# Performance work log

Hardware: AMD Instinct MI355X
Metric: run time of the kernel (lower is better)

Reference implementation:

```python
import jax, jax.numpy as jnp
import numpy as np

B, S, D = 2, 2048, 1024
M = 2048          # d_mlp
E = 8             # num_experts
TOP_K = 2


def setup_inputs() -> dict:
    key = jax.random.key(0)
    ks = jax.random.split(key, 5)
    std = 0.02
    return {
        "residual": jax.random.normal(ks[0], (B, S, D), jnp.float32),
        "W_router": jax.random.normal(ks[1], (D, E), jnp.float32) * std,
        "W_gate": jax.random.normal(ks[2], (E, D, M), jnp.float32) * std,
        "b_gate": jnp.zeros((E, M), jnp.float32),
        "W_up": jax.random.normal(ks[3], (E, D, M), jnp.float32) * std,
        "b_up": jnp.zeros((E, M), jnp.float32),
        "W_out": jax.random.normal(ks[4], (E, M, D), jnp.float32) * std,
        "b_out": jnp.zeros((E, D), jnp.float32),
    }


def reference(residual, W_router, W_gate, b_gate, W_up, b_up, W_out, b_out):
    # --- router: softmax over experts, top-k selection, renormalize ---
    router_logits = jnp.einsum('bsd,de->bse', residual, W_router)
    router_probs = jax.nn.softmax(router_logits, axis=-1)
    top_k_probs, top_k_idx = jax.lax.top_k(router_probs, TOP_K)          # [B,S,K]
    top_k_probs = top_k_probs / (jnp.sum(top_k_probs, -1, keepdims=True) + 1e-8)
    # per-expert combine weight [B,S,E]; top-k indices are unique per token
    one_hot = jax.nn.one_hot(top_k_idx, E, dtype=residual.dtype)          # [B,S,K,E]
    expert_weights = jnp.einsum('bsk,bske->bse', top_k_probs, one_hot)
    # --- each expert runs dense SwiGLU MLP on the FULL batch (compute-then-mask, as in source) ---
    gate = jax.nn.silu(jnp.einsum('bsd,edm->ebsm', residual, W_gate) + b_gate[:, None, None, :])
    up = jnp.einsum('bsd,edm->ebsm', residual, W_up) + b_up[:, None, None, :]
    hidden = gate * up                                                    # [E,B,S,M]
    expert_out = jnp.einsum('ebsm,emd->ebsd', hidden, W_out) + b_out[:, None, None, :]
    # --- weighted combine (weights are zero for non-selected experts) ---
    output = jnp.einsum('bse,ebsd->bsd', expert_weights, expert_out)
    return output
```

## Files before the change

kernel.cpp:

```cpp
#include <hip/hip_runtime.h>
#include <cstdint>
#include <cstddef>

#define TT 4096
#define DD 1024
#define MM 2048
#define EE 8
#define NPAIR 8192

typedef unsigned short u16;
typedef __bf16 bf16x8 __attribute__((ext_vector_type(8)));
typedef float f32x4 __attribute__((ext_vector_type(4)));
typedef u16 u16x8 __attribute__((ext_vector_type(8)));
typedef __attribute__((address_space(3))) void* lds_vp;
typedef __attribute__((address_space(1))) const void* gbl_cvp;

__device__ __forceinline__ void async16(u16* l, const u16* g) {
  __builtin_amdgcn_global_load_lds((gbl_cvp)(const void*)g, (lds_vp)(void*)l, 16, 0, 0);
}

__device__ __forceinline__ u16 f2bf(float f) {
  uint32_t u = __builtin_bit_cast(uint32_t, f);
  u += 0x7fffu + ((u >> 16) & 1u);
  return (u16)(u >> 16);
}
__device__ __forceinline__ float bf2f(u16 h) {
  uint32_t u = ((uint32_t)h) << 16;
  return __builtin_bit_cast(float, u);
}

__global__ void router_kernel(const float* __restrict__ X, const float* __restrict__ Wr,
                              int* __restrict__ tok_idx, float* __restrict__ wpair,
                              u16* __restrict__ Xbf) {
  int wave = threadIdx.x >> 6;
  int lane = threadIdx.x & 63;
  int t = blockIdx.x * 4 + wave;
  const float4* x4 = (const float4*)(X + (size_t)t * DD);
  float acc[EE];
#pragma unroll
  for (int e = 0; e < EE; e++) acc[e] = 0.f;
#pragma unroll
  for (int i = 0; i < 4; i++) {
    float4 xv = x4[i * 64 + lane];
    ushort4 o;
    o.x = f2bf(xv.x); o.y = f2bf(xv.y); o.z = f2bf(xv.z); o.w = f2bf(xv.w);
    *(ushort4*)&Xbf[(size_t)t * DD + (size_t)(i * 64 + lane) * 4] = o;
    const float4* wr4 = (const float4*)(Wr + (size_t)(i * 256 + lane * 4) * EE);
    float xs[4] = {xv.x, xv.y, xv.z, xv.w};
#pragma unroll
    for (int c = 0; c < 4; c++) {
      float4 wa = wr4[c * 2 + 0];
      float4 wb = wr4[c * 2 + 1];
      acc[0] += xs[c] * wa.x; acc[1] += xs[c] * wa.y;
      acc[2] += xs[c] * wa.z; acc[3] += xs[c] * wa.w;
      acc[4] += xs[c] * wb.x; acc[5] += xs[c] * wb.y;
      acc[6] += xs[c] * wb.z; acc[7] += xs[c] * wb.w;
    }
  }
#pragma unroll
  for (int off = 32; off > 0; off >>= 1)
#pragma unroll
    for (int e = 0; e < EE; e++) acc[e] += __shfl_xor(acc[e], off);
  if (lane == 0) {
    float mx = acc[0];
#pragma unroll
    for (int e = 1; e < EE; e++) mx = fmaxf(mx, acc[e]);
    float p[EE], s = 0.f;
#pragma unroll
    for (int e = 0; e < EE; e++) { p[e] = __expf(acc[e] - mx); s += p[e]; }
    float inv = 1.f / s;
#pragma unroll
    for (int e = 0; e < EE; e++) p[e] *= inv;
    int i0 = 0;
#pragma unroll
    for (int e = 1; e < EE; e++) if (p[e] > p[i0]) i0 = e;
    int i1 = (i0 == 0) ? 1 : 0;
#pragma unroll
    for (int e = 0; e < EE; e++) if (e != i0 && p[e] > p[i1]) i1 = e;
    float denom = p[i0] + p[i1] + 1e-8f;
    tok_idx[t * 2 + 0] = i0;
    tok_idx[t * 2 + 1] = i1;
    wpair[t * 2 + 0] = p[i0] / denom;
    wpair[t * 2 + 1] = p[i1] / denom;
  }
}

__global__ void bucket_kernel(const int* __restrict__ tok_idx, int* __restrict__ offsets,
                              int* __restrict__ bucket) {
  __shared__ int lcnt[EE];
  __shared__ int lcur[EE];
  int tid = threadIdx.x;
  if (tid < EE) lcnt[tid] = 0;
  __syncthreads();
  for (int i = tid; i < NPAIR; i += 1024) atomicAdd(&lcnt[tok_idx[i]], 1);
  __syncthreads();
  if (tid == 0) {
    int s = 0;
    for (int e = 0; e < EE; e++) {
      offsets[e] = s;
      lcur[e] = s;
      s += lcnt[e];
    }
    offsets[EE] = s;
  }
  __syncthreads();
  for (int i = tid; i < NPAIR; i += 1024) {
    int e = tok_idx[i];
    int pos = atomicAdd(&lcur[e], 1);
    bucket[pos] = i;
  }
}

__global__ __launch_bounds__(256)
void transpose_cvt(const float* __restrict__ in, u16* __restrict__ out, int R, int C) {
  __shared__ float tile[64][65];
  int e = blockIdx.z;
  const float* I = in + (size_t)e * R * C;
  u16* O = out + (size_t)e * R * C;
  int c0 = blockIdx.x * 64, r0 = blockIdx.y * 64;
  int t = threadIdx.x;
  {
    int cq = t & 15;
    int rb = t >> 4;
#pragma unroll
    for (int i = 0; i < 4; i++) {
      int r = rb + i * 16;
      float4 v = *(const float4*)&I[(size_t)(r0 + r) * C + c0 + cq * 4];
      tile[cq * 4 + 0][r] = v.x;
      tile[cq * 4 + 1][r] = v.y;
      tile[cq * 4 + 2][r] = v.z;
      tile[cq * 4 + 3][r] = v.w;
    }
  }
  __syncthreads();
  {
    int rseg = (t & 7) * 8;
    int cc = t >> 3;
#pragma unroll
    for (int i = 0; i < 2; i++) {
      int c = cc + i * 32;
      u16x8 o;
#pragma unroll
      for (int k = 0; k < 8; k++) o[k] = f2bf(tile[c][rseg + k]);
      *(u16x8*)&O[(size_t)(c0 + c) * R + r0 + rseg] = o;
    }
  }
}

__device__ __forceinline__ bool tile_map(const int* __restrict__ offsets, int x,
                                         int& expert, int& row0, int& rows) {
  expert = -1;
#pragma unroll 1
  for (int e = 0; e < EE; e++) {
    int o0 = offsets[e], o1 = offsets[e + 1];
    int nt = (o1 - o0 + 127) >> 7;
    if (x < nt) { expert = e; row0 = o0 + (x << 7); rows = min(128, o1 - row0); return true; }
    x -= nt;
  }
  return false;
}

template <int NTLOG2>
__device__ __forceinline__ void grid_decode(int bid, int& rt, int& n0) {
  int xcd = bid & 7, slot = bid >> 3;
  rt = xcd * 9 + (slot >> NTLOG2);
  n0 = (slot & ((1 << NTLOG2) - 1)) * 128;
}


template <int MODE>
__global__ __launch_bounds__(256)
void moe_gemm(const u16* __restrict__ Aglob, const u16* __restrict__ Wt,
              const float* __restrict__ bias, u16* __restrict__ Hws,
              float* __restrict__ Ypart, const int* __restrict__ offsets,
              const int* __restrict__ bucket, const float* __restrict__ wpair) {
  constexpr int K = (MODE == 2) ? MM : DD;
  constexpr int N = (MODE == 2) ? DD : MM;

  int rt, n0;
  grid_decode<(MODE == 2) ? 3 : 4>(blockIdx.x, rt, n0);
  int expert, row0, rows;
  if (!tile_map(offsets, rt, expert, row0, rows)) return;

  __shared__ u16 Alds[128 * 32];
  __shared__ u16 Blds[128 * 32];

  int tid = threadIdx.x;
  int wave = tid >> 6, lane = tid & 63;
  int wm = wave >> 1, wn = wave & 1;
  int quad = lane >> 4, l15 = lane & 15;
  int swz = ((lane & 3) ^ ((lane >> 3) & 3)) * 8;
  int rp  = (quad ^ ((l15 >> 1) & 3)) * 8;

  long arow0, arow1;
  {
    int r0l = wave * 32 + (lane >> 2);
    int rr0 = min(r0l, rows - 1);
    int rr1 = min(r0l + 16, rows - 1);
    if (MODE == 2) {
      arow0 = (long)(row0 + rr0) * K;
      arow1 = (long)(row0 + rr1) * K;
    } else {
      arow0 = (long)(bucket[row0 + rr0] >> 1) * K;
      arow1 = (long)(bucket[row0 + rr1] >> 1) * K;
    }
  }
  const u16* A0 = Aglob + arow0 + swz;
  const u16* A1 = Aglob + arow1 + swz;
  const u16* B0 = Wt + (size_t)expert * N * K + (size_t)n0 * K
                  + (long)(wave * 32 + (lane >> 2)) * K + swz;
  const u16* B1 = B0 + 16 * K;

  u16* sA0 = &Alds[(wave * 32) * 32]; u16* sA1 = &Alds[(wave * 32 + 16) * 32];
  u16* sB0 = &Blds[(wave * 32) * 32]; u16* sB1 = &Blds[(wave * 32 + 16) * 32];

  f32x4 acc[4][4];
#pragma unroll
  for (int i = 0; i < 4; i++)
#pragma unroll
    for (int j = 0; j < 4; j++) acc[i][j] = (f32x4){0, 0, 0, 0};

  for (int k0 = 0; k0 < K; k0 += 32) {
    async16(sA0, A0); async16(sA1, A1);
    async16(sB0, B0); async16(sB1, B1);
    A0 += 32; A1 += 32; B0 += 32; B1 += 32;
    __syncthreads();
    bf16x8 af[4], bf[4];
#pragma unroll
    for (int i = 0; i < 4; i++) {
      af[i] = *(const bf16x8*)&Alds[(wm * 64 + i * 16 + l15) * 32 + rp];
      bf[i] = *(const bf16x8*)&Blds[(wn * 64 + i * 16 + l15) * 32 + rp];
    }
#pragma unroll
    for (int i = 0; i < 4; i++)
#pragma unroll
      for (int j = 0; j < 4; j++)
        acc[i][j] = __builtin_amdgcn_mfma_f32_16x16x32_bf16(af[i], bf[j], acc[i][j], 0, 0, 0);
    __syncthreads();
  }

#pragma unroll
  for (int i = 0; i < 4; i++) {
    int lrb = wm * 64 + i * 16 + quad * 4;
#pragma unroll
    for (int j = 0; j < 4; j++) {
      int gc = n0 + wn * 64 + j * 16 + l15;
      float bv = bias[expert * N + gc];
#pragma unroll
      for (int r = 0; r < 4; r++) {
        int lr = lrb + r;
        if (lr < rows) {
          int grow = row0 + lr;
          float v = acc[i][j][r] + bv;
          if (MODE == 0) {
            Hws[(size_t)grow * MM + gc] = f2bf(v);
          } else if (MODE == 1) {
            float u = bf2f(Hws[(size_t)grow * MM + gc]);
            float sg = v / (1.f + __expf(-v));
            Hws[(size_t)grow * MM + gc] = f2bf(sg * u);
          } else {
            int p = bucket[grow];
            float w = wpair[p];
            Ypart[(size_t)p * DD + gc] = w * v;
          }
        }
      }
    }
  }
}

__global__ void combine_kernel(const float* __restrict__ Ypart, float* __restrict__ out) {
  int i = blockIdx.x * 256 + threadIdx.x;
  int t = i >> 8;
  int c4 = i & 255;
  const float4* y0 = (const float4*)(Ypart + (size_t)(2 * t) * DD) + c4;
  const float4* y1 = (const float4*)(Ypart + (size_t)(2 * t + 1) * DD) + c4;
  float4 a = *y0, b = *y1;
  float4 o;
  o.x = a.x + b.x; o.y = a.y + b.y; o.z = a.z + b.z; o.w = a.w + b.w;
  ((float4*)out)[i] = o;
}

extern "C" void kernel_launch(void* const* d_in, const int* in_sizes, int n_in,
                              void* d_out, int out_size, void* d_ws, size_t ws_size,
                              hipStream_t stream) {
  const float* residual = (const float*)d_in[0];
  const float* W_router = (const float*)d_in[1];
  const float* W_gate   = (const float*)d_in[2];
  const float* b_gate   = (const float*)d_in[3];
  const float* W_up     = (const float*)d_in[4];
  const float* b_up     = (const float*)d_in[5];
  const float* W_out    = (const float*)d_in[6];
  const float* b_out    = (const float*)d_in[7];
  float* out = (float*)d_out;

  char* ws = (char*)d_ws;
  int*   tok_idx = (int*)(ws + 0);
  float* wpair   = (float*)(ws + 32768);
  int*   offsets = (int*)(ws + 65536);
  int*   bucket  = (int*)(ws + 65536 + 512);
  u16*   Xbf  = (u16*)(ws + 131072);
  u16*   WtG  = Xbf + (size_t)TT * DD;
  u16*   WtU  = WtG + (size_t)EE * MM * DD;
  u16*   WtO  = WtU + (size_t)EE * MM * DD;
  u16*   Hws  = WtO + (size_t)EE * DD * MM;
  float* Ypart = (float*)(Hws + (size_t)NPAIR * MM);

  router_kernel<<<dim3(TT / 4), dim3(256), 0, stream>>>(residual, W_router, tok_idx, wpair, Xbf);
  bucket_kernel<<<dim3(1), dim3(1024), 0, stream>>>(tok_idx, offsets, bucket);
  transpose_cvt<<<dim3(MM / 64, DD / 64, EE), dim3(256), 0, stream>>>(W_gate, WtG, DD, MM);
  transpose_cvt<<<dim3(MM / 64, DD / 64, EE), dim3(256), 0, stream>>>(W_up,   WtU, DD, MM);
  transpose_cvt<<<dim3(DD / 64, MM / 64, EE), dim3(256), 0, stream>>>(W_out,  WtO, MM, DD);
  moe_gemm<0><<<dim3(8 * 9 * 16), dim3(256), 0, stream>>>(Xbf, WtU, b_up,   Hws, Ypart, offsets, bucket, wpair);
  moe_gemm<1><<<dim3(8 * 9 * 16), dim3(256), 0, stream>>>(Xbf, WtG, b_gate, Hws, Ypart, offsets, bucket, wpair);
  moe_gemm<2><<<dim3(8 * 9 * 8),  dim3(256), 0, stream>>>(Hws, WtO, b_out,  Hws, Ypart, offsets, bucket, wpair);
  combine_kernel<<<dim3(TT * DD / 4 / 256), dim3(256), 0, stream>>>(Ypart, out);
}
```

Baseline: 479.2 us.

## Double GEMM K-tile to 64, merge weight transposes, reorder grid decode

The MoE GEMM now stages a 64-wide K slice per iteration using an XOR swizzle over 8 chunks. That halves the number of barrier pairs per tile and doubles the MFMA work between syncs, at the cost of twice the LDS. The three weight transpose-convert launches are merged into one flat-grid kernel, which cuts launch overhead. Grid decoding now walks row tiles within an N column first, so consecutive blocks on the same XCD share weight columns in L2. The merged transpose kernel keeps a block of dead, contradictory setup code that the following block overwrites.

```diff
diff --git a/kernel.cpp b/kernel.cpp
--- a/kernel.cpp
+++ b/kernel.cpp
@@ -112,16 +112,46 @@
 }
 
 __global__ __launch_bounds__(256)
-void transpose_cvt(const float* __restrict__ in, u16* __restrict__ out, int R, int C) {
+void transpose_all(const float* __restrict__ Wg, const float* __restrict__ Wu,
+                   const float* __restrict__ Wo, u16* __restrict__ WtG,
+                   u16* __restrict__ WtU, u16* __restrict__ WtO) {
   __shared__ float tile[64][65];
-  int e = blockIdx.z;
+  int bid = blockIdx.x;
+  int mid = bid >> 9;
+  int tix = bid & 511;
+  const float* in; u16* out; int R, C, cx, ry, e;
+  if (mid < 2) {
+    in = (mid == 0) ? Wg : Wu;  out = (mid == 0) ? WtG : WtU;
+    R = DD; C = MM;
+    e = tix >> 6;
+    int t = tix & 63;
+    cx = t & 31; ry = t >> 5;
+    ry = (t >> 5) + ((tix & 63) >> 5) * 0;
+    e = tix / 512;
+    int tt = tix;
+    e = 0; (void)e;
+    cx = 0; ry = 0;
+  }
+  {
+    int m, t;
+    if (bid < 4096)       { m = 0; t = bid; }
+    else if (bid < 8192)  { m = 1; t = bid - 4096; }
+    else                  { m = 2; t = bid - 8192; }
+    if (m == 0) { in = Wg; out = WtG; R = DD; C = MM; }
+    else if (m == 1) { in = Wu; out = WtU; R = DD; C = MM; }
+    else { in = Wo; out = WtO; R = MM; C = DD; }
+    int tpe = (R >> 6) * (C >> 6);
+    e = t / tpe; t -= e * tpe;
+    int ctiles = C >> 6;
+    ry = t / ctiles; cx = t - ry * ctiles;
+  }
   const float* I = in + (size_t)e * R * C;
   u16* O = out + (size_t)e * R * C;
-  int c0 = blockIdx.x * 64, r0 = blockIdx.y * 64;
-  int t = threadIdx.x;
+  int c0 = cx * 64, r0 = ry * 64;
+  int th = threadIdx.x;
   {
-    int cq = t & 15;
-    int rb = t >> 4;
+    int cq = th & 15;
+    int rb = th >> 4;
 #pragma unroll
     for (int i = 0; i < 4; i++) {
       int r = rb + i * 16;
@@ -134,8 +164,8 @@
   }
   __syncthreads();
   {
-    int rseg = (t & 7) * 8;
-    int cc = t >> 3;
+    int rseg = (th & 7) * 8;
+    int cc = th >> 3;
 #pragma unroll
     for (int i = 0; i < 2; i++) {
       int c = cc + i * 32;
@@ -160,14 +190,6 @@
   return false;
 }
 
-template <int NTLOG2>
-__device__ __forceinline__ void grid_decode(int bid, int& rt, int& n0) {
-  int xcd = bid & 7, slot = bid >> 3;
-  rt = xcd * 9 + (slot >> NTLOG2);
-  n0 = (slot & ((1 << NTLOG2) - 1)) * 128;
-}
-
-
 template <int MODE>
 __global__ __launch_bounds__(256)
 void moe_gemm(const u16* __restrict__ Aglob, const u16* __restrict__ Wt,
@@ -177,42 +199,47 @@
   constexpr int K = (MODE == 2) ? MM : DD;
   constexpr int N = (MODE == 2) ? DD : MM;
 
-  int rt, n0;
-  grid_decode<(MODE == 2) ? 3 : 4>(blockIdx.x, rt, n0);
+  int bid = blockIdx.x;
+  int xcd = bid & 7, slot = bid >> 3;
+  int n0i = slot / 9;
+  int rloc = slot - n0i * 9;
+  int rt = xcd * 9 + rloc;
+  int n0 = n0i * 128;
+
   int expert, row0, rows;
   if (!tile_map(offsets, rt, expert, row0, rows)) return;
 
-  __shared__ u16 Alds[128 * 32];
-  __shared__ u16 Blds[128 * 32];
+  __shared__ u16 Alds[128 * 64];
+  __shared__ u16 Blds[128 * 64];
 
   int tid = threadIdx.x;
   int wave = tid >> 6, lane = tid & 63;
   int wm = wave >> 1, wn = wave & 1;
   int quad = lane >> 4, l15 = lane & 15;
-  int swz = ((lane & 3) ^ ((lane >> 3) & 3)) * 8;
-  int rp  = (quad ^ ((l15 >> 1) & 3)) * 8;
-
-  long arow0, arow1;
-  {
-    int r0l = wave * 32 + (lane >> 2);
-    int rr0 = min(r0l, rows - 1);
-    int rr1 = min(r0l + 16, rows - 1);
-    if (MODE == 2) {
-      arow0 = (long)(row0 + rr0) * K;
-      arow1 = (long)(row0 + rr1) * K;
-    } else {
-      arow0 = (long)(bucket[row0 + rr0] >> 1) * K;
-      arow1 = (long)(bucket[row0 + rr1] >> 1) * K;
-    }
-  }
-  const u16* A0 = Aglob + arow0 + swz;
-  const u16* A1 = Aglob + arow1 + swz;
-  const u16* B0 = Wt + (size_t)expert * N * K + (size_t)n0 * K
-                  + (long)(wave * 32 + (lane >> 2)) * K + swz;
-  const u16* B1 = B0 + 16 * K;
-
-  u16* sA0 = &Alds[(wave * 32) * 32]; u16* sA1 = &Alds[(wave * 32 + 16) * 32];
-  u16* sB0 = &Blds[(wave * 32) * 32]; u16* sB1 = &Blds[(wave * 32 + 16) * 32];
+  int rl8 = lane >> 3;
+  int src_c = ((lane & 7) ^ rl8) * 8;
+
+  const u16* Aptr[4];
+  const u16* Bptr[4];
+  u16* sA[4];
+  u16* sB[4];
+  const u16* Wbase = Wt + (size_t)expert * N * K + (size_t)n0 * K;
+#pragma unroll
+  for (int j = 0; j < 4; j++) {
+    int r = wave * 32 + j * 8 + rl8;
+    int rr = min(r, rows - 1);
+    long arow;
+    if (MODE == 2) arow = (long)(row0 + rr) * K;
+    else           arow = (long)(bucket[row0 + rr] >> 1) * K;
+    Aptr[j] = Aglob + arow + src_c;
+    Bptr[j] = Wbase + (long)r * K + src_c;
+    sA[j] = &Alds[(wave * 32 + j * 8) * 64];
+    sB[j] = &Blds[(wave * 32 + j * 8) * 64];
+  }
+
+  int pbase = (quad ^ (l15 & 7)) * 8;
+  int arow_f = wm * 64 + l15;
+  int brow_f = wn * 64 + l15;
 
   f32x4 acc[4][4];
 #pragma unroll
@@ -220,22 +247,29 @@
 #pragma unroll
     for (int j = 0; j < 4; j++) acc[i][j] = (f32x4){0, 0, 0, 0};
 
-  for (int k0 = 0; k0 < K; k0 += 32) {
-    async16(sA0, A0); async16(sA1, A1);
-    async16(sB0, B0); async16(sB1, B1);
-    A0 += 32; A1 += 32; B0 += 32; B1 += 32;
+  for (int k0 = 0; k0 < K; k0 += 64) {
+#pragma unroll
+    for (int j = 0; j < 4; j++) {
+      async16(sA[j], Aptr[j]);
+      async16(sB[j], Bptr[j]);
+      Aptr[j] += 64; Bptr[j] += 64;
+    }
     __syncthreads();
-    bf16x8 af[4], bf[4];
-#pragma unroll
-    for (int i = 0; i < 4; i++) {
-      af[i] = *(const bf16x8*)&Alds[(wm * 64 + i * 16 + l15) * 32 + rp];
-      bf[i] = *(const bf16x8*)&Blds[(wn * 64 + i * 16 + l15) * 32 + rp];
-    }
-#pragma unroll
-    for (int i = 0; i < 4; i++)
-#pragma unroll
-      for (int j = 0; j < 4; j++)
-        acc[i][j] = __builtin_amdgcn_mfma_f32_16x16x32_bf16(af[i], bf[j], acc[i][j], 0, 0, 0);
+#pragma unroll
+    for (int s = 0; s < 2; s++) {
+      int poff = pbase ^ (s * 32);
+      bf16x8 af[4], bf[4];
+#pragma unroll
+      for (int i = 0; i < 4; i++) {
+        af[i] = *(const bf16x8*)&Alds[(arow_f + i * 16) * 64 + poff];
+        bf[i] = *(const bf16x8*)&Blds[(brow_f + i * 16) * 64 + poff];
+      }
+#pragma unroll
+      for (int i = 0; i < 4; i++)
+#pragma unroll
+        for (int j = 0; j < 4; j++)
+          acc[i][j] = __builtin_amdgcn_mfma_f32_16x16x32_bf16(af[i], bf[j], acc[i][j], 0, 0, 0);
+    }
     __syncthreads();
   }
 
@@ -308,11 +342,9 @@
 
   router_kernel<<<dim3(TT / 4), dim3(256), 0, stream>>>(residual, W_router, tok_idx, wpair, Xbf);
   bucket_kernel<<<dim3(1), dim3(1024), 0, stream>>>(tok_idx, offsets, bucket);
-  transpose_cvt<<<dim3(MM / 64, DD / 64, EE), dim3(256), 0, stream>>>(W_gate, WtG, DD, MM);
-  transpose_cvt<<<dim3(MM / 64, DD / 64, EE), dim3(256), 0, stream>>>(W_up,   WtU, DD, MM);
-  transpose_cvt<<<dim3(DD / 64, MM / 64, EE), dim3(256), 0, stream>>>(W_out,  WtO, MM, DD);
-  moe_gemm<0><<<dim3(8 * 9 * 16), dim3(256), 0, stream>>>(Xbf, WtU, b_up,   Hws, Ypart, offsets, bucket, wpair);
-  moe_gemm<1><<<dim3(8 * 9 * 16), dim3(256), 0, stream>>>(Xbf, WtG, b_gate, Hws, Ypart, offsets, bucket, wpair);
-  moe_gemm<2><<<dim3(8 * 9 * 8),  dim3(256), 0, stream>>>(Hws, WtO, b_out,  Hws, Ypart, offsets, bucket, wpair);
+  transpose_all<<<dim3(3 * 4096), dim3(256), 0, stream>>>(W_gate, W_up, W_out, WtG, WtU, WtO);
+  moe_gemm<0><<<dim3(8 * 16 * 9), dim3(256), 0, stream>>>(Xbf, WtU, b_up,   Hws, Ypart, offsets, bucket, wpair);
+  moe_gemm<1><<<dim3(8 * 16 * 9), dim3(256), 0, stream>>>(Xbf, WtG, b_gate, Hws, Ypart, offsets, bucket, wpair);
+  moe_gemm<2><<<dim3(8 * 8 * 9),  dim3(256), 0, stream>>>(Hws, WtO, b_out,  Hws, Ypart, offsets, bucket, wpair);
   combine_kernel<<<dim3(TT * DD / 4 / 256), dim3(256), 0, stream>>>(Ypart, out);
 }
```

Result: slower. 540.5 us (+12.8%).
